# Performance work log

Hardware: AMD Instinct MI355X
Metric: run time of the kernel (lower is better)

## Reference

```python
import jax, jax.numpy as jnp
import numpy as np

H = 768


def _glorot(key, shape):
    fan_in = shape[-1]
    return jax.random.normal(key, shape, dtype=jnp.float32) / np.sqrt(fan_in)


def setup_inputs() -> dict:
    key = jax.random.key(0)
    ks = jax.random.split(key, 12)
    B, L, K, Lg = 8, 256, 32, 128
    return {
        "x": jax.random.normal(ks[0], (B, L, H), dtype=jnp.float32),
        "s": jax.random.normal(ks[1], (B, K, H), dtype=jnp.float32),
        "g": jax.random.normal(ks[2], (B, Lg, H), dtype=jnp.float32),
        "Wq": _glorot(ks[3], (H, H)),
        "bq": jnp.zeros((H,), jnp.float32),
        "Wkv": _glorot(ks[4], (2 * H, H)),
        "bkv": jnp.zeros((2 * H,), jnp.float32),
        "Wg1": _glorot(ks[5], (H, 2 * H)),
        "bg1": jnp.zeros((H,), jnp.float32),
        "Wg2": _glorot(ks[6], (H, 2 * H)),
        "bg2": jnp.zeros((H,), jnp.float32),
    }


def _gate(xb, yb, W, b):
    # gate = sigmoid(Linear(concat([x, y], -1))) using split-weight trick:
    # concat([x,y]) @ W.T = x @ Wx.T + y @ Wy.T  (avoids materializing 2H concat)
    Wx, Wy = W[:, :H], W[:, H:]
    gate = jax.nn.sigmoid(jnp.einsum('blkh,oh->blko', xb, Wx)
                          + jnp.einsum('blkh,oh->blko', yb, Wy) + b)
    return gate * xb + (1.0 - gate) * yb


def reference(x, s, g, Wq, bq, Wkv, bkv, Wg1, bg1, Wg2, bg2):
    B, L, _ = x.shape
    K = s.shape[1]
    q = jnp.einsum('blh,oh->blo', x, Wq) + bq                    # (B,L,H)
    kv = jnp.einsum('bmh,oh->bmo', g, Wkv) + bkv                 # (B,Lg,2H)
    k, v = kv[..., :H], kv[..., H:]
    scores = jnp.einsum('blh,bmh->blm', q, k) / np.sqrt(H)       # (B,L,Lg)
    scores = jax.nn.softmax(scores, axis=-1)
    gctx = jnp.einsum('blm,bmh->blh', scores, v)                 # (B,L,H)
    # broadcast to (B,L,K,H)
    gb = jnp.broadcast_to(gctx[:, :, None, :], (B, L, K, H))
    hb = jnp.broadcast_to(x[:, :, None, :], (B, L, K, H))
    sb = jnp.broadcast_to(s[:, None, :, :], (B, L, K, H))
    h = _gate(hb, gb, Wg1, bg1)
    h = _gate(h, sb, Wg2, bg2)
    return h
```

## Files before the change

kernel.cpp:

```cpp
#include <hip/hip_runtime.h>
#include <math.h>

#define Hd 768
#define Bb 8
#define Ll 256
#define Kk 32
#define LG 128

using half4 = __attribute__((ext_vector_type(4))) _Float16;
using half8 = __attribute__((ext_vector_type(8))) _Float16;
using f32x4 = __attribute__((ext_vector_type(4))) float;

struct ConvArgs {
    const float* src[8];
    _Float16*    dst[8];
    int cum[9];
    int sstr[8];
    int dstr[8];
    int rl[8];
};

__global__ __launch_bounds__(256) void conv_multi(ConvArgs a) {
    int c = blockIdx.x * 256 + threadIdx.x;
    if (c >= a.cum[8]) return;
    int s = 0;
    while (c >= a.cum[s + 1]) ++s;
    const int lc  = c - a.cum[s];
    const unsigned cpr = (unsigned)(a.rl[s] >> 3);
    const unsigned row = (unsigned)lc / cpr;
    const int col = (lc - (int)(row * cpr)) * 8;
    const float* sp = a.src[s] + (size_t)row * a.sstr[s] + col;
    float4 v0 = *(const float4*)sp;
    float4 v1 = *(const float4*)(sp + 4);
    half8 h;
    h[0] = (_Float16)v0.x; h[1] = (_Float16)v0.y; h[2] = (_Float16)v0.z; h[3] = (_Float16)v0.w;
    h[4] = (_Float16)v1.x; h[5] = (_Float16)v1.y; h[6] = (_Float16)v1.z; h[7] = (_Float16)v1.w;
    *(half8*)(a.dst[s] + (size_t)row * a.dstr[s] + col) = h;
}

__global__ __launch_bounds__(256) void gemm_f16(
    const _Float16* __restrict__ A, int lda, long sA,
    const _Float16* __restrict__ W, int ldw, long sW,
    const float* __restrict__ bias,
    float* __restrict__ C, int ldc, long sC,
    _Float16* __restrict__ C2, int ldc2, long sC2,
    int Kd, int kvsplit,
    _Float16* __restrict__ K16, _Float16* __restrict__ VT16)
{
    __shared__ _Float16 As[128][72];
    __shared__ _Float16 Ws[64][72];

    const int t    = threadIdx.x;
    const int w    = t >> 6;
    const int lane = t & 63;
    const int quad = lane >> 4;
    const int l16  = lane & 15;
    const int bm   = blockIdx.y * 128;
    const int bn   = blockIdx.x * 64;
    const int z    = blockIdx.z;
    A += (size_t)z * sA;
    W += (size_t)z * sW;

    const int sr = t >> 3;
    const int sk = (t & 7) * 8;

    f32x4 acc[2][4] = {};

    for (int k0 = 0; k0 < Kd; k0 += 64) {
        half8 av[4], wv[2];
        #pragma unroll
        for (int i = 0; i < 4; ++i)
            av[i] = *(const half8*)(A + (size_t)(bm + i * 32 + sr) * lda + k0 + sk);
        #pragma unroll
        for (int i = 0; i < 2; ++i)
            wv[i] = *(const half8*)(W + (size_t)(bn + i * 32 + sr) * ldw + k0 + sk);
        __syncthreads();
        #pragma unroll
        for (int i = 0; i < 4; ++i) *(half8*)&As[i * 32 + sr][sk] = av[i];
        #pragma unroll
        for (int i = 0; i < 2; ++i) *(half8*)&Ws[i * 32 + sr][sk] = wv[i];
        __syncthreads();
        #pragma unroll
        for (int kk = 0; kk < 2; ++kk) {
            half8 af[2], bf[4];
            af[0] = *(const half8*)&As[w * 32 + l16][kk * 32 + quad * 8];
            af[1] = *(const half8*)&As[w * 32 + 16 + l16][kk * 32 + quad * 8];
            #pragma unroll
            for (int j = 0; j < 4; ++j)
                bf[j] = *(const half8*)&Ws[j * 16 + l16][kk * 32 + quad * 8];
            #pragma unroll
            for (int rt = 0; rt < 2; ++rt)
                #pragma unroll
                for (int j = 0; j < 4; ++j)
                    acc[rt][j] = __builtin_amdgcn_mfma_f32_16x16x32_f16(
                        af[rt], bf[j], acc[rt][j], 0, 0, 0);
        }
    }

    #pragma unroll
    for (int rt = 0; rt < 2; ++rt) {
        #pragma unroll
        for (int j = 0; j < 4; ++j) {
            const int col  = bn + j * 16 + l16;
            const int row0 = bm + w * 32 + rt * 16 + quad * 4;
            const float bv = bias ? bias[col] : 0.f;
            if (kvsplit) {
                if (col < 768) {
                    #pragma unroll
                    for (int r = 0; r < 4; ++r)
                        K16[(size_t)(row0 + r) * 768 + col] = (_Float16)(acc[rt][j][r] + bv);
                } else {
                    const int b = row0 >> 7, h = col - 768, m0 = row0 & 127;
                    half4 hv;
                    #pragma unroll
                    for (int r = 0; r < 4; ++r) hv[r] = (_Float16)(acc[rt][j][r] + bv);
                    *(half4*)(VT16 + ((size_t)(b * 768 + h)) * 128 + m0) = hv;
                }
            } else {
                #pragma unroll
                for (int r = 0; r < 4; ++r) {
                    const float v = acc[rt][j][r] + bv;
                    const size_t rr = (size_t)(row0 + r);
                    if (C)  C[(size_t)z * sC + rr * ldc + col] = v;
                    if (C2) C2[(size_t)z * sC2 + rr * ldc2 + col] = (_Float16)v;
                }
            }
        }
    }
}

__global__ __launch_bounds__(256) void softmax_rows(
    const float* __restrict__ sc, _Float16* __restrict__ P)
{
    const int wave = threadIdx.x >> 6, lane = threadIdx.x & 63;
    const int r = blockIdx.x * 4 + wave;
    const float* row = sc + (size_t)r * 128;
    const float scale = 0.03608439182435161f;
    float a = row[lane] * scale, b = row[lane + 64] * scale;
    float mx = fmaxf(a, b);
    #pragma unroll
    for (int off = 32; off; off >>= 1) mx = fmaxf(mx, __shfl_xor(mx, off, 64));
    float e0 = __expf(a - mx), e1 = __expf(b - mx);
    float s = e0 + e1;
    #pragma unroll
    for (int off = 32; off; off >>= 1) s += __shfl_xor(s, off, 64);
    const float inv = 1.f / s;
    P[(size_t)r * 128 + lane]      = (_Float16)(e0 * inv);
    P[(size_t)r * 128 + lane + 64] = (_Float16)(e1 * inv);
}

__device__ __forceinline__ float sigm(float z) { return 1.f / (1.f + __expf(-z)); }

__global__ __launch_bounds__(256) void gate1_combine(
    const float4* __restrict__ t1, const float4* __restrict__ x,
    const float4* __restrict__ gc, float4* __restrict__ h1,
    _Float16* __restrict__ h16)
{
    const int i = blockIdx.x * 256 + threadIdx.x;
    float4 z = t1[i], xv = x[i], gv = gc[i];
    float4 o;
    float g;
    g = sigm(z.x); o.x = g * xv.x + (1.f - g) * gv.x;
    g = sigm(z.y); o.y = g * xv.y + (1.f - g) * gv.y;
    g = sigm(z.z); o.z = g * xv.z + (1.f - g) * gv.z;
    g = sigm(z.w); o.w = g * xv.w + (1.f - g) * gv.w;
    h1[i] = o;
    half4 h;
    h[0] = (_Float16)o.x; h[1] = (_Float16)o.y; h[2] = (_Float16)o.z; h[3] = (_Float16)o.w;
    *(half4*)(h16 + (size_t)i * 4) = h;
}

__global__ __launch_bounds__(256) void final_combine(
    const float4* __restrict__ D, const float4* __restrict__ E,
    const float4* __restrict__ h1, const float4* __restrict__ s,
    float4* __restrict__ out)
{
    const int f   = blockIdx.x * 256 + threadIdx.x;
    const int h4  = f % 192;
    const int row = f / 192;
    const int k   = row & 31;
    const int bl  = row >> 5;
    const int b   = bl >> 8;
    const int bk  = b * Kk + k;

    float4 d  = D[bl * 192 + h4];
    float4 e  = E[bk * 192 + h4];
    float4 hv = h1[bl * 192 + h4];
    float4 sv = s[bk * 192 + h4];
    float4 o;
    float g;
    g = sigm(d.x + e.x); o.x = g * hv.x + (1.f - g) * sv.x;
    g = sigm(d.y + e.y); o.y = g * hv.y + (1.f - g) * sv.y;
    g = sigm(d.z + e.z); o.z = g * hv.z + (1.f - g) * sv.z;
    g = sigm(d.w + e.w); o.w = g * hv.w + (1.f - g) * sv.w;
    out[f] = o;
}

extern "C" void kernel_launch(void* const* d_in, const int* in_sizes, int n_in,
                              void* d_out, int out_size, void* d_ws, size_t ws_size,
                              hipStream_t stream) {
    const float* x   = (const float*)d_in[0];
    const float* s   = (const float*)d_in[1];
    const float* g   = (const float*)d_in[2];
    const float* Wq  = (const float*)d_in[3];
    const float* bq  = (const float*)d_in[4];
    const float* Wkv = (const float*)d_in[5];
    const float* bkv = (const float*)d_in[6];
    const float* Wg1 = (const float*)d_in[7];
    const float* bg1 = (const float*)d_in[8];
    const float* Wg2 = (const float*)d_in[9];
    const float* bg2 = (const float*)d_in[10];

    char* w = (char*)d_ws;
    float* bufA = (float*)(w);
    float* bufB = (float*)(w + 6291456);
    float* bufC = (float*)(w + 12582912);
    float* sc32 = (float*)(w);
    _Float16* P16 = (_Float16*)(w + 1048576);
    _Float16* xg16   = (_Float16*)(w + 18874368);
    _Float16* g16    = (_Float16*)(w + 25165824);
    _Float16* s16    = (_Float16*)(w + 26738688);
    _Float16* q16    = (_Float16*)(w + 27131904);
    _Float16* h116   = (_Float16*)(w + 27131904);
    _Float16* k16    = (_Float16*)(w + 30277632);
    float*    bufE   = (float*)(w + 30277632);
    _Float16* vT16   = (_Float16*)(w + 31850496);
    _Float16* Wq16   = (_Float16*)(w + 6291456);
    _Float16* Wkv16  = (_Float16*)(w + 7471104);
    _Float16* Wg116  = (_Float16*)(w + 9830400);
    _Float16* Wg2a16 = (_Float16*)(w + 33423360);
    _Float16* Wg2b16 = (_Float16*)(w + 34603008);
    float* out = (float*)d_out;

    const dim3 blk(256);

    ConvArgs ca;
    ca.src[0] = x;         ca.dst[0] = xg16;   ca.sstr[0] = 768;  ca.dstr[0] = 1536; ca.rl[0] = 768;
    ca.src[1] = g;         ca.dst[1] = g16;    ca.sstr[1] = 768;  ca.dstr[1] = 768;  ca.rl[1] = 768;
    ca.src[2] = s;         ca.dst[2] = s16;    ca.sstr[2] = 768;  ca.dstr[2] = 768;  ca.rl[2] = 768;
    ca.src[3] = Wq;        ca.dst[3] = Wq16;   ca.sstr[3] = 768;  ca.dstr[3] = 768;  ca.rl[3] = 768;
    ca.src[4] = Wkv;       ca.dst[4] = Wkv16;  ca.sstr[4] = 768;  ca.dstr[4] = 768;  ca.rl[4] = 768;
    ca.src[5] = Wg1;       ca.dst[5] = Wg116;  ca.sstr[5] = 1536; ca.dstr[5] = 1536; ca.rl[5] = 1536;
    ca.src[6] = Wg2;       ca.dst[6] = Wg2a16; ca.sstr[6] = 1536; ca.dstr[6] = 768;  ca.rl[6] = 768;
    ca.src[7] = Wg2 + 768; ca.dst[7] = Wg2b16; ca.sstr[7] = 1536; ca.dstr[7] = 768;  ca.rl[7] = 768;
    ca.cum[0] = 0;      ca.cum[1] = 196608; ca.cum[2] = 294912; ca.cum[3] = 319488;
    ca.cum[4] = 393216; ca.cum[5] = 540672; ca.cum[6] = 688128; ca.cum[7] = 761856;
    ca.cum[8] = 835584;
    conv_multi<<<dim3(3264), blk, 0, stream>>>(ca);

    gemm_f16<<<dim3(12, 16, 1), blk, 0, stream>>>(
        xg16, 1536, 0, Wq16, 768, 0, bq,
        nullptr, 0, 0, q16, 768, 0, 768, 0, nullptr, nullptr);
    gemm_f16<<<dim3(24, 8, 1), blk, 0, stream>>>(
        g16, 768, 0, Wkv16, 768, 0, bkv,
        nullptr, 0, 0, nullptr, 0, 0, 768, 1, k16, vT16);
    gemm_f16<<<dim3(2, 2, 8), blk, 0, stream>>>(
        q16, 768, 256L * 768, k16, 768, 128L * 768, nullptr,
        sc32, 128, 256L * 128, nullptr, 0, 0, 768, 0, nullptr, nullptr);
    softmax_rows<<<dim3(512), blk, 0, stream>>>(sc32, P16);
    gemm_f16<<<dim3(12, 2, 8), blk, 0, stream>>>(
        P16, 128, 256L * 128, vT16, 128, 768L * 128, nullptr,
        bufC, 768, 256L * 768, xg16 + 768, 1536, 256L * 1536, 128, 0, nullptr, nullptr);
    gemm_f16<<<dim3(12, 16, 1), blk, 0, stream>>>(
        xg16, 1536, 0, Wg116, 1536, 0, bg1,
        bufA, 768, 0, nullptr, 0, 0, 1536, 0, nullptr, nullptr);
    gate1_combine<<<dim3(1536), blk, 0, stream>>>(
        (const float4*)bufA, (const float4*)x, (const float4*)bufC, (float4*)bufB, h116);
    gemm_f16<<<dim3(12, 16, 1), blk, 0, stream>>>(
        h116, 768, 0, Wg2a16, 768, 0, bg2,
        bufA, 768, 0, nullptr, 0, 0, 768, 0, nullptr, nullptr);
    gemm_f16<<<dim3(12, 2, 1), blk, 0, stream>>>(
        s16, 768, 0, Wg2b16, 768, 0, nullptr,
        bufE, 768, 0, nullptr, 0, 0, 768, 0, nullptr, nullptr);
    final_combine<<<dim3(49152), blk, 0, stream>>>(
        (const float4*)bufA, (const float4*)bufE, (const float4*)bufB,
        (const float4*)s, (float4*)out);
}
```

Before: 356.2 us.

## Fuse gating epilogues into GEMMs, fuse scores with softmax, batch independent GEMMs

Combines the Q, KV and s-projection GEMMs into one multi-descriptor launch and fuses the attention score GEMM with the row softmax. The gate1 sigmoid-combine moves into the Wg1 GEMM epilogue, and the final gate with its K-broadcast output write moves into the Wg2a GEMM epilogue. This removes launches and intermediate fp32 round trips through global memory. In exchange, the large output write is now done by only 192 blocks, which may limit memory-level parallelism.

```diff
diff --git a/kernel.cpp b/kernel.cpp
--- a/kernel.cpp
+++ b/kernel.cpp
@@ -10,6 +10,8 @@
 using half4 = __attribute__((ext_vector_type(4))) _Float16;
 using half8 = __attribute__((ext_vector_type(8))) _Float16;
 using f32x4 = __attribute__((ext_vector_type(4))) float;
+
+__device__ __forceinline__ float sigm(float z) { return 1.f / (1.f + __expf(-z)); }
 
 struct ConvArgs {
     const float* src[8];
@@ -129,71 +131,363 @@
     }
 }
 
-__global__ __launch_bounds__(256) void softmax_rows(
-    const float* __restrict__ sc, _Float16* __restrict__ P)
+struct G3Desc {
+    const _Float16* A;
+    const _Float16* W;
+    const float* bias;
+    void* o0;
+    void* o1;
+    int lda, ldw, mode, nbx;
+};
+struct G3Args { G3Desc d[3]; int cum[4]; };
+
+__global__ __launch_bounds__(256) void gemm3(G3Args ga) {
+    __shared__ _Float16 As[128][72];
+    __shared__ _Float16 Ws[64][72];
+
+    const int t    = threadIdx.x;
+    const int w    = t >> 6;
+    const int lane = t & 63;
+    const int quad = lane >> 4;
+    const int l16  = lane & 15;
+
+    int s = 0;
+    const int bid = blockIdx.x;
+    while (bid >= ga.cum[s + 1]) ++s;
+    const int local = bid - ga.cum[s];
+    const int nbx   = ga.d[s].nbx;
+    const int by    = local / nbx;
+    const int bx    = local - by * nbx;
+    const int bm    = by * 128;
+    const int bn    = bx * 64;
+    const _Float16* A = ga.d[s].A;
+    const _Float16* W = ga.d[s].W;
+    const int lda = ga.d[s].lda;
+    const int ldw = ga.d[s].ldw;
+
+    const int sr = t >> 3;
+    const int sk = (t & 7) * 8;
+
+    f32x4 acc[2][4] = {};
+
+    for (int k0 = 0; k0 < 768; k0 += 64) {
+        half8 av[4], wv[2];
+        #pragma unroll
+        for (int i = 0; i < 4; ++i)
+            av[i] = *(const half8*)(A + (size_t)(bm + i * 32 + sr) * lda + k0 + sk);
+        #pragma unroll
+        for (int i = 0; i < 2; ++i)
+            wv[i] = *(const half8*)(W + (size_t)(bn + i * 32 + sr) * ldw + k0 + sk);
+        __syncthreads();
+        #pragma unroll
+        for (int i = 0; i < 4; ++i) *(half8*)&As[i * 32 + sr][sk] = av[i];
+        #pragma unroll
+        for (int i = 0; i < 2; ++i) *(half8*)&Ws[i * 32 + sr][sk] = wv[i];
+        __syncthreads();
+        #pragma unroll
+        for (int kk = 0; kk < 2; ++kk) {
+            half8 af[2], bf[4];
+            af[0] = *(const half8*)&As[w * 32 + l16][kk * 32 + quad * 8];
+            af[1] = *(const half8*)&As[w * 32 + 16 + l16][kk * 32 + quad * 8];
+            #pragma unroll
+            for (int j = 0; j < 4; ++j)
+                bf[j] = *(const half8*)&Ws[j * 16 + l16][kk * 32 + quad * 8];
+            #pragma unroll
+            for (int rt = 0; rt < 2; ++rt)
+                #pragma unroll
+                for (int j = 0; j < 4; ++j)
+                    acc[rt][j] = __builtin_amdgcn_mfma_f32_16x16x32_f16(
+                        af[rt], bf[j], acc[rt][j], 0, 0, 0);
+        }
+    }
+
+    const int mode = ga.d[s].mode;
+    const float* bias = ga.d[s].bias;
+    #pragma unroll
+    for (int rt = 0; rt < 2; ++rt) {
+        #pragma unroll
+        for (int j = 0; j < 4; ++j) {
+            const int col  = bn + j * 16 + l16;
+            const int row0 = bm + w * 32 + rt * 16 + quad * 4;
+            const float bv = bias ? bias[col] : 0.f;
+            if (mode == 0) {
+                _Float16* C2 = (_Float16*)ga.d[s].o0;
+                #pragma unroll
+                for (int r = 0; r < 4; ++r)
+                    C2[(size_t)(row0 + r) * 768 + col] = (_Float16)(acc[rt][j][r] + bv);
+            } else if (mode == 1) {
+                _Float16* K16  = (_Float16*)ga.d[s].o0;
+                _Float16* VT16 = (_Float16*)ga.d[s].o1;
+                if (col < 768) {
+                    #pragma unroll
+                    for (int r = 0; r < 4; ++r)
+                        K16[(size_t)(row0 + r) * 768 + col] = (_Float16)(acc[rt][j][r] + bv);
+                } else {
+                    const int b = row0 >> 7, h = col - 768, m0 = row0 & 127;
+                    half4 hv;
+                    #pragma unroll
+                    for (int r = 0; r < 4; ++r) hv[r] = (_Float16)(acc[rt][j][r] + bv);
+                    *(half4*)(VT16 + ((size_t)(b * 768 + h)) * 128 + m0) = hv;
+                }
+            } else {
+                float* C = (float*)ga.d[s].o0;
+                #pragma unroll
+                for (int r = 0; r < 4; ++r)
+                    C[(size_t)(row0 + r) * 768 + col] = acc[rt][j][r] + bv;
+            }
+        }
+    }
+}
+
+__global__ __launch_bounds__(256) void attn_scores_sm(
+    const _Float16* __restrict__ Q, const _Float16* __restrict__ Kt,
+    _Float16* __restrict__ P)
 {
-    const int wave = threadIdx.x >> 6, lane = threadIdx.x & 63;
-    const int r = blockIdx.x * 4 + wave;
-    const float* row = sc + (size_t)r * 128;
+    __shared__ _Float16 As[64][72];
+    __shared__ _Float16 Ws[128][72];
+
+    const int t    = threadIdx.x;
+    const int w    = t >> 6;
+    const int lane = t & 63;
+    const int quad = lane >> 4;
+    const int l16  = lane & 15;
+    const int z    = blockIdx.y;
+    const int bm   = blockIdx.x * 64;
+    const _Float16* A = Q  + (size_t)z * 256 * 768 + (size_t)bm * 768;
+    const _Float16* W = Kt + (size_t)z * 128 * 768;
+
+    const int sr = t >> 3;
+    const int sk = (t & 7) * 8;
+
+    f32x4 acc[8] = {};
+
+    for (int k0 = 0; k0 < 768; k0 += 64) {
+        half8 av[2], wv[4];
+        #pragma unroll
+        for (int i = 0; i < 2; ++i)
+            av[i] = *(const half8*)(A + (size_t)(i * 32 + sr) * 768 + k0 + sk);
+        #pragma unroll
+        for (int i = 0; i < 4; ++i)
+            wv[i] = *(const half8*)(W + (size_t)(i * 32 + sr) * 768 + k0 + sk);
+        __syncthreads();
+        #pragma unroll
+        for (int i = 0; i < 2; ++i) *(half8*)&As[i * 32 + sr][sk] = av[i];
+        #pragma unroll
+        for (int i = 0; i < 4; ++i) *(half8*)&Ws[i * 32 + sr][sk] = wv[i];
+        __syncthreads();
+        #pragma unroll
+        for (int kk = 0; kk < 2; ++kk) {
+            half8 af = *(const half8*)&As[w * 16 + l16][kk * 32 + quad * 8];
+            #pragma unroll
+            for (int j = 0; j < 8; ++j) {
+                half8 bf = *(const half8*)&Ws[j * 16 + l16][kk * 32 + quad * 8];
+                acc[j] = __builtin_amdgcn_mfma_f32_16x16x32_f16(af, bf, acc[j], 0, 0, 0);
+            }
+        }
+    }
+
     const float scale = 0.03608439182435161f;
-    float a = row[lane] * scale, b = row[lane + 64] * scale;
-    float mx = fmaxf(a, b);
-    #pragma unroll
-    for (int off = 32; off; off >>= 1) mx = fmaxf(mx, __shfl_xor(mx, off, 64));
-    float e0 = __expf(a - mx), e1 = __expf(b - mx);
-    float s = e0 + e1;
-    #pragma unroll
-    for (int off = 32; off; off >>= 1) s += __shfl_xor(s, off, 64);
-    const float inv = 1.f / s;
-    P[(size_t)r * 128 + lane]      = (_Float16)(e0 * inv);
-    P[(size_t)r * 128 + lane + 64] = (_Float16)(e1 * inv);
-}
-
-__device__ __forceinline__ float sigm(float z) { return 1.f / (1.f + __expf(-z)); }
-
-__global__ __launch_bounds__(256) void gate1_combine(
-    const float4* __restrict__ t1, const float4* __restrict__ x,
-    const float4* __restrict__ gc, float4* __restrict__ h1,
-    _Float16* __restrict__ h16)
+    #pragma unroll
+    for (int r = 0; r < 4; ++r) {
+        float v[8];
+        float mx = -1e30f;
+        #pragma unroll
+        for (int j = 0; j < 8; ++j) { v[j] = acc[j][r] * scale; mx = fmaxf(mx, v[j]); }
+        #pragma unroll
+        for (int off = 8; off; off >>= 1) mx = fmaxf(mx, __shfl_xor(mx, off, 16));
+        float sum = 0.f;
+        #pragma unroll
+        for (int j = 0; j < 8; ++j) { v[j] = __expf(v[j] - mx); sum += v[j]; }
+        #pragma unroll
+        for (int off = 8; off; off >>= 1) sum += __shfl_xor(sum, off, 16);
+        const float inv = 1.f / sum;
+        const int row = bm + w * 16 + quad * 4 + r;
+        _Float16* Pr = P + (size_t)z * 256 * 128 + (size_t)row * 128;
+        #pragma unroll
+        for (int j = 0; j < 8; ++j) Pr[j * 16 + l16] = (_Float16)(v[j] * inv);
+    }
+}
+
+__global__ __launch_bounds__(256) void gemm_gate1(
+    const _Float16* __restrict__ A,
+    const _Float16* __restrict__ W,
+    const float* __restrict__ bias,
+    const float* __restrict__ X,
+    const float* __restrict__ GC,
+    float* __restrict__ H1,
+    _Float16* __restrict__ H16)
 {
-    const int i = blockIdx.x * 256 + threadIdx.x;
-    float4 z = t1[i], xv = x[i], gv = gc[i];
-    float4 o;
-    float g;
-    g = sigm(z.x); o.x = g * xv.x + (1.f - g) * gv.x;
-    g = sigm(z.y); o.y = g * xv.y + (1.f - g) * gv.y;
-    g = sigm(z.z); o.z = g * xv.z + (1.f - g) * gv.z;
-    g = sigm(z.w); o.w = g * xv.w + (1.f - g) * gv.w;
-    h1[i] = o;
-    half4 h;
-    h[0] = (_Float16)o.x; h[1] = (_Float16)o.y; h[2] = (_Float16)o.z; h[3] = (_Float16)o.w;
-    *(half4*)(h16 + (size_t)i * 4) = h;
-}
-
-__global__ __launch_bounds__(256) void final_combine(
-    const float4* __restrict__ D, const float4* __restrict__ E,
-    const float4* __restrict__ h1, const float4* __restrict__ s,
-    float4* __restrict__ out)
+    __shared__ _Float16 As[128][72];
+    __shared__ _Float16 Ws[64][72];
+
+    const int t    = threadIdx.x;
+    const int w    = t >> 6;
+    const int lane = t & 63;
+    const int quad = lane >> 4;
+    const int l16  = lane & 15;
+    const int bm   = blockIdx.y * 128;
+    const int bn   = blockIdx.x * 64;
+
+    const int sr = t >> 3;
+    const int sk = (t & 7) * 8;
+
+    f32x4 acc[2][4] = {};
+
+    for (int k0 = 0; k0 < 1536; k0 += 64) {
+        half8 av[4], wv[2];
+        #pragma unroll
+        for (int i = 0; i < 4; ++i)
+            av[i] = *(const half8*)(A + (size_t)(bm + i * 32 + sr) * 1536 + k0 + sk);
+        #pragma unroll
+        for (int i = 0; i < 2; ++i)
+            wv[i] = *(const half8*)(W + (size_t)(bn + i * 32 + sr) * 1536 + k0 + sk);
+        __syncthreads();
+        #pragma unroll
+        for (int i = 0; i < 4; ++i) *(half8*)&As[i * 32 + sr][sk] = av[i];
+        #pragma unroll
+        for (int i = 0; i < 2; ++i) *(half8*)&Ws[i * 32 + sr][sk] = wv[i];
+        __syncthreads();
+        #pragma unroll
+        for (int kk = 0; kk < 2; ++kk) {
+            half8 af[2], bf[4];
+            af[0] = *(const half8*)&As[w * 32 + l16][kk * 32 + quad * 8];
+            af[1] = *(const half8*)&As[w * 32 + 16 + l16][kk * 32 + quad * 8];
+            #pragma unroll
+            for (int j = 0; j < 4; ++j)
+                bf[j] = *(const half8*)&Ws[j * 16 + l16][kk * 32 + quad * 8];
+            #pragma unroll
+            for (int rt = 0; rt < 2; ++rt)
+                #pragma unroll
+                for (int j = 0; j < 4; ++j)
+                    acc[rt][j] = __builtin_amdgcn_mfma_f32_16x16x32_f16(
+                        af[rt], bf[j], acc[rt][j], 0, 0, 0);
+        }
+    }
+
+    #pragma unroll
+    for (int rt = 0; rt < 2; ++rt) {
+        #pragma unroll
+        for (int j = 0; j < 4; ++j) {
+            const int col  = bn + j * 16 + l16;
+            const int row0 = bm + w * 32 + rt * 16 + quad * 4;
+            const float bv = bias[col];
+            #pragma unroll
+            for (int r = 0; r < 4; ++r) {
+                const size_t off = (size_t)(row0 + r) * 768 + col;
+                const float g = sigm(acc[rt][j][r] + bv);
+                const float o = g * X[off] + (1.f - g) * GC[off];
+                H1[off]  = o;
+                H16[off] = (_Float16)o;
+            }
+        }
+    }
+}
+
+__global__ __launch_bounds__(256) void gemm_final(
+    const _Float16* __restrict__ A,
+    const _Float16* __restrict__ W,
+    const float* __restrict__ bias,
+    const float* __restrict__ Ebuf,
+    const float* __restrict__ Sbuf,
+    const float* __restrict__ H1,
+    float* __restrict__ out)
 {
-    const int f   = blockIdx.x * 256 + threadIdx.x;
-    const int h4  = f % 192;
-    const int row = f / 192;
-    const int k   = row & 31;
-    const int bl  = row >> 5;
-    const int b   = bl >> 8;
-    const int bk  = b * Kk + k;
-
-    float4 d  = D[bl * 192 + h4];
-    float4 e  = E[bk * 192 + h4];
-    float4 hv = h1[bl * 192 + h4];
-    float4 sv = s[bk * 192 + h4];
-    float4 o;
-    float g;
-    g = sigm(d.x + e.x); o.x = g * hv.x + (1.f - g) * sv.x;
-    g = sigm(d.y + e.y); o.y = g * hv.y + (1.f - g) * sv.y;
-    g = sigm(d.z + e.z); o.z = g * hv.z + (1.f - g) * sv.z;
-    g = sigm(d.w + e.w); o.w = g * hv.w + (1.f - g) * sv.w;
-    out[f] = o;
+    __shared__ union {
+        struct { _Float16 As[128][72]; _Float16 Ws[64][72]; } a;
+        float Ds[128][76];
+    } u;
+    __shared__ float Es[32][64];
+    __shared__ float Ss[32][64];
+
+    const int t    = threadIdx.x;
+    const int w    = t >> 6;
+    const int lane = t & 63;
+    const int quad = lane >> 4;
+    const int l16  = lane & 15;
+    const int bm   = blockIdx.y * 128;
+    const int bn   = blockIdx.x * 64;
+    const int bK   = (bm >> 8) * 32;
+
+    const int sr = t >> 3;
+    const int sk = (t & 7) * 8;
+
+    #pragma unroll
+    for (int i = 0; i < 2; ++i) {
+        const int idx = t + i * 256;
+        const int k = idx >> 4, c = (idx & 15) * 4;
+        *(float4*)&Es[k][c] = *(const float4*)(Ebuf + (size_t)(bK + k) * 768 + bn + c);
+        *(float4*)&Ss[k][c] = *(const float4*)(Sbuf + (size_t)(bK + k) * 768 + bn + c);
+    }
+
+    f32x4 acc[2][4] = {};
+
+    for (int k0 = 0; k0 < 768; k0 += 64) {
+        half8 av[4], wv[2];
+        #pragma unroll
+        for (int i = 0; i < 4; ++i)
+            av[i] = *(const half8*)(A + (size_t)(bm + i * 32 + sr) * 768 + k0 + sk);
+        #pragma unroll
+        for (int i = 0; i < 2; ++i)
+            wv[i] = *(const half8*)(W + (size_t)(bn + i * 32 + sr) * 768 + k0 + sk);
+        __syncthreads();
+        #pragma unroll
+        for (int i = 0; i < 4; ++i) *(half8*)&u.a.As[i * 32 + sr][sk] = av[i];
+        #pragma unroll
+        for (int i = 0; i < 2; ++i) *(half8*)&u.a.Ws[i * 32 + sr][sk] = wv[i];
+        __syncthreads();
+        #pragma unroll
+        for (int kk = 0; kk < 2; ++kk) {
+            half8 af[2], bf[4];
+            af[0] = *(const half8*)&u.a.As[w * 32 + l16][kk * 32 + quad * 8];
+            af[1] = *(const half8*)&u.a.As[w * 32 + 16 + l16][kk * 32 + quad * 8];
+            #pragma unroll
+            for (int j = 0; j < 4; ++j)
+                bf[j] = *(const half8*)&u.a.Ws[j * 16 + l16][kk * 32 + quad * 8];
+            #pragma unroll
+            for (int rt = 0; rt < 2; ++rt)
+                #pragma unroll
+                for (int j = 0; j < 4; ++j)
+                    acc[rt][j] = __builtin_amdgcn_mfma_f32_16x16x32_f16(
+                        af[rt], bf[j], acc[rt][j], 0, 0, 0);
+        }
+    }
+
+    __syncthreads();
+    #pragma unroll
+    for (int rt = 0; rt < 2; ++rt) {
+        #pragma unroll
+        for (int j = 0; j < 4; ++j) {
+            const int col = j * 16 + l16;
+            const float bv = bias[bn + col];
+            #pragma unroll
+            for (int r = 0; r < 4; ++r)
+                u.Ds[w * 32 + rt * 16 + quad * 4 + r][col] = acc[rt][j][r] + bv;
+        }
+    }
+    __syncthreads();
+
+    const int c  = (t & 15) * 4;
+    const int r0 = (t >> 4) * 8;
+    float4 d[8], h[8];
+    #pragma unroll
+    for (int rr = 0; rr < 8; ++rr) {
+        d[rr] = *(const float4*)&u.Ds[r0 + rr][c];
+        h[rr] = *(const float4*)(H1 + (size_t)(bm + r0 + rr) * 768 + bn + c);
+    }
+    float* ob = out + (size_t)(bm + r0) * 32 * 768 + bn + c;
+    for (int k = 0; k < 32; ++k) {
+        const float4 e  = *(const float4*)&Es[k][c];
+        const float4 sv = *(const float4*)&Ss[k][c];
+        #pragma unroll
+        for (int rr = 0; rr < 8; ++rr) {
+            float4 o; float g;
+            g = sigm(d[rr].x + e.x); o.x = g * h[rr].x + (1.f - g) * sv.x;
+            g = sigm(d[rr].y + e.y); o.y = g * h[rr].y + (1.f - g) * sv.y;
+            g = sigm(d[rr].z + e.z); o.z = g * h[rr].z + (1.f - g) * sv.z;
+            g = sigm(d[rr].w + e.w); o.w = g * h[rr].w + (1.f - g) * sv.w;
+            *(float4*)(ob + (size_t)(rr * 32 + k) * 768) = o;
+        }
+    }
 }
 
 extern "C" void kernel_launch(void* const* d_in, const int* in_sizes, int n_in,
@@ -212,24 +506,22 @@
     const float* bg2 = (const float*)d_in[10];
 
     char* w = (char*)d_ws;
-    float* bufA = (float*)(w);
-    float* bufB = (float*)(w + 6291456);
-    float* bufC = (float*)(w + 12582912);
-    float* sc32 = (float*)(w);
-    _Float16* P16 = (_Float16*)(w + 1048576);
-    _Float16* xg16   = (_Float16*)(w + 18874368);
-    _Float16* g16    = (_Float16*)(w + 25165824);
-    _Float16* s16    = (_Float16*)(w + 26738688);
-    _Float16* q16    = (_Float16*)(w + 27131904);
-    _Float16* h116   = (_Float16*)(w + 27131904);
-    _Float16* k16    = (_Float16*)(w + 30277632);
-    float*    bufE   = (float*)(w + 30277632);
-    _Float16* vT16   = (_Float16*)(w + 31850496);
-    _Float16* Wq16   = (_Float16*)(w + 6291456);
-    _Float16* Wkv16  = (_Float16*)(w + 7471104);
-    _Float16* Wg116  = (_Float16*)(w + 9830400);
-    _Float16* Wg2a16 = (_Float16*)(w + 33423360);
-    _Float16* Wg2b16 = (_Float16*)(w + 34603008);
+    _Float16* P16    = (_Float16*)(w + 0);
+    _Float16* xg16   = (_Float16*)(w + 524288);
+    _Float16* g16    = (_Float16*)(w + 6815744);
+    _Float16* s16    = (_Float16*)(w + 8388608);
+    _Float16* q16    = (_Float16*)(w + 8781824);
+    _Float16* k16    = (_Float16*)(w + 11927552);
+    _Float16* vT16   = (_Float16*)(w + 13500416);
+    _Float16* Wq16   = (_Float16*)(w + 15073280);
+    _Float16* Wkv16  = (_Float16*)(w + 16252928);
+    _Float16* Wg116  = (_Float16*)(w + 18612224);
+    _Float16* Wg2a16 = (_Float16*)(w + 20971520);
+    _Float16* Wg2b16 = (_Float16*)(w + 22151168);
+    float*    bufE   = (float*)(w + 23330816);
+    float*    bufC   = (float*)(w + 24117248);
+    float*    bufB   = (float*)(w + 30408704);
+    _Float16* h116   = (_Float16*)(w + 36700160);
     float* out = (float*)d_out;
 
     const dim3 blk(256);
@@ -248,31 +540,22 @@
     ca.cum[8] = 835584;
     conv_multi<<<dim3(3264), blk, 0, stream>>>(ca);
 
-    gemm_f16<<<dim3(12, 16, 1), blk, 0, stream>>>(
-        xg16, 1536, 0, Wq16, 768, 0, bq,
-        nullptr, 0, 0, q16, 768, 0, 768, 0, nullptr, nullptr);
-    gemm_f16<<<dim3(24, 8, 1), blk, 0, stream>>>(
-        g16, 768, 0, Wkv16, 768, 0, bkv,
-        nullptr, 0, 0, nullptr, 0, 0, 768, 1, k16, vT16);
-    gemm_f16<<<dim3(2, 2, 8), blk, 0, stream>>>(
-        q16, 768, 256L * 768, k16, 768, 128L * 768, nullptr,
-        sc32, 128, 256L * 128, nullptr, 0, 0, 768, 0, nullptr, nullptr);
-    softmax_rows<<<dim3(512), blk, 0, stream>>>(sc32, P16);
+    G3Args ga = {};
+    ga.d[0] = { xg16, Wq16,   bq,      (void*)q16,  nullptr,     1536, 768, 0, 12 };
+    ga.d[1] = { g16,  Wkv16,  bkv,     (void*)k16,  (void*)vT16, 768,  768, 1, 24 };
+    ga.d[2] = { s16,  Wg2b16, nullptr, (void*)bufE, nullptr,     768,  768, 2, 12 };
+    ga.cum[0] = 0; ga.cum[1] = 192; ga.cum[2] = 384; ga.cum[3] = 408;
+    gemm3<<<dim3(408), blk, 0, stream>>>(ga);
+
+    attn_scores_sm<<<dim3(4, 8), blk, 0, stream>>>(q16, k16, P16);
+
     gemm_f16<<<dim3(12, 2, 8), blk, 0, stream>>>(
         P16, 128, 256L * 128, vT16, 128, 768L * 128, nullptr,
         bufC, 768, 256L * 768, xg16 + 768, 1536, 256L * 1536, 128, 0, nullptr, nullptr);
-    gemm_f16<<<dim3(12, 16, 1), blk, 0, stream>>>(
-        xg16, 1536, 0, Wg116, 1536, 0, bg1,
-        bufA, 768, 0, nullptr, 0, 0, 1536, 0, nullptr, nullptr);
-    gate1_combine<<<dim3(1536), blk, 0, stream>>>(
-        (const float4*)bufA, (const float4*)x, (const float4*)bufC, (float4*)bufB, h116);
-    gemm_f16<<<dim3(12, 16, 1), blk, 0, stream>>>(
-        h116, 768, 0, Wg2a16, 768, 0, bg2,
-        bufA, 768, 0, nullptr, 0, 0, 768, 0, nullptr, nullptr);
-    gemm_f16<<<dim3(12, 2, 1), blk, 0, stream>>>(
-        s16, 768, 0, Wg2b16, 768, 0, nullptr,
-        bufE, 768, 0, nullptr, 0, 0, 768, 0, nullptr, nullptr);
-    final_combine<<<dim3(49152), blk, 0, stream>>>(
-        (const float4*)bufA, (const float4*)bufE, (const float4*)bufB,
-        (const float4*)s, (float4*)out);
-}
+
+    gemm_gate1<<<dim3(12, 16), blk, 0, stream>>>(
+        xg16, Wg116, bg1, x, bufC, bufB, h116);
+
+    gemm_final<<<dim3(12, 16), blk, 0, stream>>>(
+        h116, Wg2a16, bg2, bufE, s, bufB, out);
+}
```

After: 322.3 us. -9.5%, faster.
